# Performance work log

Hardware: AMD Instinct MI355X
Metric: run time of the kernel (lower is better)

The kernel has to match this reference:

```python
import jax, jax.numpy as jnp
import numpy as np
import math

B, L, D, H = 2, 2048, 1024, 16
HD = D // H
DILATION, WINDOW, CAUSAL = 2, 512, True
EPS = 1e-5  # nn.LayerNorm default


def _ln(x, g, b):
    mu = x.mean(-1, keepdims=True)
    var = ((x - mu) ** 2).mean(-1, keepdims=True)
    return (x - mu) * jax.lax.rsqrt(var + EPS) * g + b


def setup_inputs() -> dict:
    key = jax.random.key(0)
    ks = jax.random.split(key, 8)
    s = 0.02  # small init scale to keep activations sane
    return {
        'x': jax.random.normal(ks[0], (B, L, D), jnp.float32),
        'ln1_g': jnp.ones((D,), jnp.float32),
        'ln1_b': jnp.zeros((D,), jnp.float32),
        'Wqkv': jax.random.normal(ks[1], (D, 3 * D), jnp.float32) * s,
        'bqkv': jnp.zeros((3 * D,), jnp.float32),
        'Wout': jax.random.normal(ks[2], (D, D), jnp.float32) * s,
        'bout': jnp.zeros((D,), jnp.float32),
        'ln2_g': jnp.ones((D,), jnp.float32),
        'ln2_b': jnp.zeros((D,), jnp.float32),
        'W1': jax.random.normal(ks[3], (D, 4 * D), jnp.float32) * s,
        'b1': jnp.zeros((4 * D,), jnp.float32),
        'W2': jax.random.normal(ks[4], (4 * D, D), jnp.float32) * s,
        'b2': jnp.zeros((D,), jnp.float32),
    }


def _keep_mask():
    # True = allowed. Matches _build_dilated_keep_mask.
    idx = jnp.arange(L, dtype=jnp.int32)
    delta = idx[:, None] - idx[None, :]
    keep = (jnp.remainder(delta, DILATION) == 0)
    keep = keep & (jnp.abs(delta) <= WINDOW)
    if CAUSAL:
        keep = keep & (delta >= 0)
    return keep  # [L, L]


def reference(x, ln1_g, ln1_b, Wqkv, bqkv, Wout, bout, ln2_g, ln2_b, W1, b1, W2, b2):
    # --- attention sub-block (pre-norm) ---
    h = _ln(x, ln1_g, ln1_b)                          # [B,L,D]
    qkv = (h @ Wqkv + bqkv).reshape(B, L, 3, H, HD)
    q = qkv[:, :, 0].transpose(0, 2, 1, 3)            # [B,H,L,HD]
    k = qkv[:, :, 1].transpose(0, 2, 1, 3)
    v = qkv[:, :, 2].transpose(0, 2, 1, 3)
    scale = 1.0 / math.sqrt(HD)
    scores = jnp.einsum('bhqd,bhkd->bhqk', q, k) * scale
    keep = _keep_mask()                               # [L,L] broadcast over B,H
    scores = jnp.where(keep, scores, jnp.float32(-1e30))
    attn = jax.nn.softmax(scores, axis=-1)
    o = jnp.einsum('bhqk,bhkd->bhqd', attn, v)        # [B,H,L,HD]
    o = o.transpose(0, 2, 1, 3).reshape(B, L, D)
    x = x + (o @ Wout + bout)
    # --- FFN sub-block (pre-norm) ---
    h2 = _ln(x, ln2_g, ln2_b)
    f = jax.nn.gelu(h2 @ W1 + b1, approximate=False)  # nn.GELU default = exact
    x = x + (f @ W2 + b2)
    return x
```

## Files before the change

kernel.cpp:

```cpp
#include <hip/hip_runtime.h>

typedef unsigned short u16;
typedef short short8 __attribute__((ext_vector_type(8)));
typedef float floatx4 __attribute__((ext_vector_type(4)));

#define B_  2
#define L_  2048
#define D_  1024
#define H_  16
#define HD_ 64
#define M_  (B_*L_)
#define LP_ 1024
#define WP_ 256

__device__ __forceinline__ float b2f(u16 u) {
    union { unsigned int i; float f; } c; c.i = ((unsigned int)u) << 16; return c.f;
}
__device__ __forceinline__ u16 f2b(float f) {
    union { float f; unsigned int i; } c; c.f = f;
    unsigned int u = c.i;
    u = u + 0x7FFFu + ((u >> 16) & 1u);
    return (u16)(u >> 16);
}
__device__ __forceinline__ float ldrawf(const void* p, size_t i, bool isbf16) {
    return isbf16 ? b2f(((const u16*)p)[i]) : ((const float*)p)[i];
}
__device__ __forceinline__ u16 ldraw16(const void* p, size_t i, bool isbf16) {
    return isbf16 ? ((const u16*)p)[i] : f2b(((const float*)p)[i]);
}

__global__ void probe_k(const u16* x, int* flag) {
    int t = threadIdx.x;
    unsigned int u = x[2 * t];
    unsigned int e = (u >> 7) & 0xFF;
    bool sane = (e >= 100 && e <= 140);
    unsigned long long m = __ballot(sane);
    if (t == 0) *flag = (__popcll(m) >= 32) ? 1 : 0;
}

__global__ __launch_bounds__(256) void transpose_k(const void* __restrict__ in,
                                                   u16* __restrict__ out, int K, int N,
                                                   const int* flagp) {
    bool isb = (*flagp != 0);
    __shared__ u16 tile[32][33];
    int tx = threadIdx.x & 31;
    int ty = threadIdx.x >> 5;
    int nb = blockIdx.x * 32;
    int kb = blockIdx.y * 32;
    #pragma unroll
    for (int j = 0; j < 32; j += 8)
        tile[ty + j][tx] = ldraw16(in, (size_t)(kb + ty + j) * N + nb + tx, isb);
    __syncthreads();
    #pragma unroll
    for (int j = 0; j < 32; j += 8)
        out[(size_t)(nb + ty + j) * K + kb + tx] = tile[tx][ty + j];
}

template<int SRC>
__global__ __launch_bounds__(256) void ln_k(const void* __restrict__ x, const void* __restrict__ g,
                                            const void* __restrict__ bb, u16* __restrict__ out,
                                            const int* flagp) {
    bool isb = (*flagp != 0);
    int row = blockIdx.x;
    int t = threadIdx.x;
    float v[4]; float s = 0.f, s2 = 0.f;
    #pragma unroll
    for (int i = 0; i < 4; i++) {
        size_t idx = (size_t)row * D_ + t + 256 * i;
        float f = (SRC == 1) ? ((const float*)x)[idx] : ldrawf(x, idx, isb);
        v[i] = f; s += f; s2 += f * f;
    }
    #pragma unroll
    for (int off = 32; off >= 1; off >>= 1) { s += __shfl_xor(s, off); s2 += __shfl_xor(s2, off); }
    __shared__ float red[8];
    int wave = t >> 6;
    if ((t & 63) == 0) { red[wave] = s; red[4 + wave] = s2; }
    __syncthreads();
    s  = red[0] + red[1] + red[2] + red[3];
    s2 = red[4] + red[5] + red[6] + red[7];
    float mu  = s * (1.0f / 1024.0f);
    float var = s2 * (1.0f / 1024.0f) - mu * mu;
    float rs  = rsqrtf(var + 1e-5f);
    #pragma unroll
    for (int i = 0; i < 4; i++) {
        int c = t + 256 * i;
        out[(size_t)row * D_ + c] = f2b((v[i] - mu) * rs * ldrawf(g, c, isb) + ldrawf(bb, c, isb));
    }
}

template<int OUT, int RES, int GELU>
__global__ __launch_bounds__(256) void gemm_k(const u16* __restrict__ A,
                                              const u16* __restrict__ BT,
                                              const void* __restrict__ bias,
                                              const void* __restrict__ resid,
                                              void* __restrict__ C,
                                              int M, int N, int K,
                                              const int* flagp) {
    bool isb = (*flagp != 0);
    __shared__ __align__(16) u16 a_s[64 * 40];
    __shared__ __align__(16) u16 b_s[64 * 40];

    const int bm = blockIdx.y, bn = blockIdx.x;
    const int t = threadIdx.x;
    const int wave = t >> 6, lane = t & 63;
    const int wm = wave >> 1, wn = wave & 1;
    const int quad = lane >> 4, r16 = lane & 15;

    const int srow = t >> 2;
    const int scol = (t & 3) * 8;

    floatx4 acc[2][2] = {};

    const u16* Ap  = A  + (size_t)(bm * 64 + srow) * K + scol;
    const u16* BTp = BT + (size_t)(bn * 64 + srow) * K + scol;

    for (int kc = 0; kc < K; kc += 32) {
        int4 av = *(const int4*)(Ap + kc);
        int4 bv = *(const int4*)(BTp + kc);
        __syncthreads();
        *(int4*)(a_s + srow * 40 + scol) = av;
        *(int4*)(b_s + srow * 40 + scol) = bv;
        __syncthreads();
        short8 af0 = *(const short8*)(a_s + (wm * 32 +      r16) * 40 + quad * 8);
        short8 af1 = *(const short8*)(a_s + (wm * 32 + 16 + r16) * 40 + quad * 8);
        short8 bf0 = *(const short8*)(b_s + (wn * 32 +      r16) * 40 + quad * 8);
        short8 bf1 = *(const short8*)(b_s + (wn * 32 + 16 + r16) * 40 + quad * 8);
        acc[0][0] = __builtin_amdgcn_mfma_f32_16x16x32_bf16(af0, bf0, acc[0][0], 0, 0, 0);
        acc[0][1] = __builtin_amdgcn_mfma_f32_16x16x32_bf16(af0, bf1, acc[0][1], 0, 0, 0);
        acc[1][0] = __builtin_amdgcn_mfma_f32_16x16x32_bf16(af1, bf0, acc[1][0], 0, 0, 0);
        acc[1][1] = __builtin_amdgcn_mfma_f32_16x16x32_bf16(af1, bf1, acc[1][1], 0, 0, 0);
    }

    #pragma unroll
    for (int mt = 0; mt < 2; mt++)
      #pragma unroll
      for (int nt = 0; nt < 2; nt++)
        #pragma unroll
        for (int r = 0; r < 4; r++) {
            int row = bm * 64 + wm * 32 + mt * 16 + quad * 4 + r;
            int col = bn * 64 + wn * 32 + nt * 16 + r16;
            float v = acc[mt][nt][r] + ldrawf(bias, col, isb);
            if (GELU) v = 0.5f * v * (1.0f + erff(v * 0.70710678118654752f));
            if (RES == 1) v += ldrawf(resid, (size_t)row * N + col, isb);
            if (RES == 2) v += ((const float*)resid)[(size_t)row * N + col];
            size_t oi = (size_t)row * N + col;
            if (OUT == 0) ((float*)C)[oi] = v;
            else if (OUT == 1) ((u16*)C)[oi] = f2b(v);
            else {
                if (isb) ((u16*)C)[oi] = f2b(v);
                else     ((float*)C)[oi] = v;
            }
        }
}

__global__ __launch_bounds__(256) void repack_k(const u16* __restrict__ qkv,
                                                u16* __restrict__ Qp, u16* __restrict__ Kp,
                                                u16* __restrict__ Vt) {
    int pid = blockIdx.x;
    int lt  = blockIdx.y;
    int b = pid >> 5, p = (pid >> 4) & 1, h = pid & 15;
    int t = threadIdx.x;
    int srow = t >> 2;
    int scol = (t & 3) * 16;

    int lp = lt * 64 + srow;
    int l  = 2 * lp + p;
    const u16* src = qkv + ((size_t)b * L_ + l) * (3 * D_) + h * HD_;
    size_t dst = ((size_t)pid * LP_ + lp) * HD_;

    *(int4*)(Qp + dst + scol)     = *(const int4*)(src + scol);
    *(int4*)(Qp + dst + scol + 8) = *(const int4*)(src + scol + 8);
    *(int4*)(Kp + dst + scol)     = *(const int4*)(src + D_ + scol);
    *(int4*)(Kp + dst + scol + 8) = *(const int4*)(src + D_ + scol + 8);

    __shared__ u16 vt[64][72];
    *(int4*)(&vt[srow][scol])     = *(const int4*)(src + 2 * D_ + scol);
    *(int4*)(&vt[srow][scol + 8]) = *(const int4*)(src + 2 * D_ + scol + 8);
    __syncthreads();
    union { u16 s[16]; int4 v[2]; } tmp;
    #pragma unroll
    for (int jj = 0; jj < 16; jj++) tmp.s[jj] = vt[scol + jj][srow];
    u16* vdst = Vt + ((size_t)pid * HD_ + srow) * LP_ + lt * 64 + scol;
    *(int4*)(vdst)     = tmp.v[0];
    *(int4*)(vdst + 8) = tmp.v[1];
}

#define FS 72
__global__ __launch_bounds__(256) void fattn_k(const u16* __restrict__ Qp,
                                               const u16* __restrict__ Kp,
                                               const u16* __restrict__ Vt,
                                               u16* __restrict__ o) {
    __shared__ __align__(16) u16 Qs[64 * FS];
    __shared__ __align__(16) u16 Ks[64 * FS];
    __shared__ __align__(16) u16 Vs[64 * FS];
    __shared__ __align__(16) u16 Ps[4][16 * FS];

    const int pid = blockIdx.x, qt = blockIdx.y;
    const int b = pid >> 5, p = (pid >> 4) & 1, h = pid & 15;
    const int t = threadIdx.x, w = t >> 6, lane = t & 63;
    const int quad = lane >> 4, r16 = lane & 15;
    const int q0 = qt * 64;

    const int srow = t >> 2;
    const int scol = (t & 3) * 16;

    const u16* qsrc = Qp + ((size_t)pid * LP_ + q0 + srow) * HD_;
    *(int4*)(Qs + srow * FS + scol)     = *(const int4*)(qsrc + scol);
    *(int4*)(Qs + srow * FS + scol + 8) = *(const int4*)(qsrc + scol + 8);
    __syncthreads();

    const short8 qf0 = *(const short8*)(Qs + (w * 16 + r16) * FS + quad * 8);
    const short8 qf1 = *(const short8*)(Qs + (w * 16 + r16) * FS + quad * 8 + 32);

    floatx4 oacc[4] = {};
    float mrow[4] = {-INFINITY, -INFINITY, -INFINITY, -INFINITY};
    float lrow[4] = {};

    const int kt0 = (qt >= 4) ? qt - 4 : 0;
    const int qrow_base = q0 + w * 16 + quad * 4;

    for (int kt = kt0; kt <= qt; ++kt) {
        __syncthreads();
        const u16* ksrc = Kp + ((size_t)pid * LP_ + kt * 64 + srow) * HD_;
        *(int4*)(Ks + srow * FS + scol)     = *(const int4*)(ksrc + scol);
        *(int4*)(Ks + srow * FS + scol + 8) = *(const int4*)(ksrc + scol + 8);
        const u16* vsrc = Vt + ((size_t)pid * HD_ + srow) * LP_ + kt * 64;
        *(int4*)(Vs + srow * FS + scol)     = *(const int4*)(vsrc + scol);
        *(int4*)(Vs + srow * FS + scol + 8) = *(const int4*)(vsrc + scol + 8);
        __syncthreads();

        floatx4 s4[4];
        #pragma unroll
        for (int nt = 0; nt < 4; nt++) {
            short8 kf0 = *(const short8*)(Ks + (nt * 16 + r16) * FS + quad * 8);
            short8 kf1 = *(const short8*)(Ks + (nt * 16 + r16) * FS + quad * 8 + 32);
            floatx4 z = {};
            z = __builtin_amdgcn_mfma_f32_16x16x32_bf16(qf0, kf0, z, 0, 0, 0);
            z = __builtin_amdgcn_mfma_f32_16x16x32_bf16(qf1, kf1, z, 0, 0, 0);
            s4[nt] = z;
        }

        float sv[4][4];
        #pragma unroll
        for (int nt = 0; nt < 4; nt++) {
            int kcol = kt * 64 + nt * 16 + r16;
            #pragma unroll
            for (int r = 0; r < 4; r++) {
                int kq = kcol - (qrow_base + r);
                bool valid = (kq <= 0) && (kq >= -WP_);
                sv[nt][r] = valid ? s4[nt][r] * 0.125f : -1e30f;
            }
        }

        float mx[4];
        #pragma unroll
        for (int r = 0; r < 4; r++)
            mx[r] = fmaxf(fmaxf(sv[0][r], sv[1][r]), fmaxf(sv[2][r], sv[3][r]));
        #pragma unroll
        for (int off = 8; off >= 1; off >>= 1)
            #pragma unroll
            for (int r = 0; r < 4; r++) mx[r] = fmaxf(mx[r], __shfl_xor(mx[r], off));

        float al[4];
        #pragma unroll
        for (int r = 0; r < 4; r++) {
            float mnew = fmaxf(mrow[r], mx[r]);
            al[r] = __expf(mrow[r] - mnew);
            mrow[r] = mnew;
        }

        float ps[4][4], rs[4] = {};
        #pragma unroll
        for (int nt = 0; nt < 4; nt++)
            #pragma unroll
            for (int r = 0; r < 4; r++) {
                float pv = __expf(sv[nt][r] - mrow[r]);
                ps[nt][r] = pv; rs[r] += pv;
            }
        #pragma unroll
        for (int off = 8; off >= 1; off >>= 1)
            #pragma unroll
            for (int r = 0; r < 4; r++) rs[r] += __shfl_xor(rs[r], off);
        #pragma unroll
        for (int r = 0; r < 4; r++) lrow[r] = lrow[r] * al[r] + rs[r];
        #pragma unroll
        for (int nt = 0; nt < 4; nt++)
            #pragma unroll
            for (int r = 0; r < 4; r++) oacc[nt][r] *= al[r];

        #pragma unroll
        for (int nt = 0; nt < 4; nt++)
            #pragma unroll
            for (int r = 0; r < 4; r++)
                Ps[w][(quad * 4 + r) * FS + nt * 16 + r16] = f2b(ps[nt][r]);
        short8 pf0 = *(const short8*)(&Ps[w][r16 * FS + quad * 8]);
        short8 pf1 = *(const short8*)(&Ps[w][r16 * FS + quad * 8 + 32]);

        #pragma unroll
        for (int nt = 0; nt < 4; nt++) {
            short8 vf0 = *(const short8*)(Vs + (nt * 16 + r16) * FS + quad * 8);
            short8 vf1 = *(const short8*)(Vs + (nt * 16 + r16) * FS + quad * 8 + 32);
            oacc[nt] = __builtin_amdgcn_mfma_f32_16x16x32_bf16(pf0, vf0, oacc[nt], 0, 0, 0);
            oacc[nt] = __builtin_amdgcn_mfma_f32_16x16x32_bf16(pf1, vf1, oacc[nt], 0, 0, 0);
        }
    }

    float inv[4];
    #pragma unroll
    for (int r = 0; r < 4; r++) inv[r] = 1.0f / lrow[r];
    #pragma unroll
    for (int nt = 0; nt < 4; nt++)
        #pragma unroll
        for (int r = 0; r < 4; r++) {
            int qp = qrow_base + r;
            int l  = 2 * qp + p;
            int d  = nt * 16 + r16;
            o[((size_t)b * L_ + l) * D_ + h * HD_ + d] = f2b(oacc[nt][r] * inv[r]);
        }
}

extern "C" void kernel_launch(void* const* d_in, const int* in_sizes, int n_in,
                              void* d_out, int out_size, void* d_ws, size_t ws_size,
                              hipStream_t stream) {
    (void)in_sizes; (void)n_in; (void)out_size; (void)ws_size;
    const void* x     = d_in[0];
    const void* ln1_g = d_in[1];
    const void* ln1_b = d_in[2];
    const void* Wqkv  = d_in[3];
    const void* bqkv  = d_in[4];
    const void* Wout  = d_in[5];
    const void* bout  = d_in[6];
    const void* ln2_g = d_in[7];
    const void* ln2_b = d_in[8];
    const void* W1    = d_in[9];
    const void* b1    = d_in[10];
    const void* W2    = d_in[11];
    const void* b2    = d_in[12];

    char* ws = (char*)d_ws;
    const size_t MB = 1024 * 1024;
    u16*   wqkvT = (u16*)ws;
    u16*   qkv   = (u16*)(ws + 6  * MB);
    u16*   woutT = (u16*)(ws + 30 * MB);
    u16*   fbuf  = (u16*)ws;
    u16*   w1T   = (u16*)(ws + 32 * MB);
    u16*   w2T   = (u16*)(ws + 40 * MB);
    u16*   bufA  = (u16*)(ws + 48 * MB);
    float* x1    = (float*)(ws + 56 * MB);
    u16*   Qp    = (u16*)(ws + 72 * MB);
    u16*   Kp    = (u16*)(ws + 80 * MB);
    u16*   Vt    = (u16*)(ws + 88 * MB);
    int*   flag  = (int*)(ws + 96 * MB);

    dim3 tb(256);
    probe_k<<<1, 64, 0, stream>>>((const u16*)x, flag);

    transpose_k<<<dim3(3 * D_ / 32, D_ / 32), tb, 0, stream>>>(Wqkv, wqkvT, D_, 3 * D_, flag);
    transpose_k<<<dim3(D_ / 32, D_ / 32), tb, 0, stream>>>(Wout, woutT, D_, D_, flag);
    transpose_k<<<dim3(4 * D_ / 32, D_ / 32), tb, 0, stream>>>(W1, w1T, D_, 4 * D_, flag);
    transpose_k<<<dim3(D_ / 32, 4 * D_ / 32), tb, 0, stream>>>(W2, w2T, 4 * D_, D_, flag);

    ln_k<0><<<M_, tb, 0, stream>>>(x, ln1_g, ln1_b, bufA, flag);

    gemm_k<1, 0, 0><<<dim3(3 * D_ / 64, M_ / 64), tb, 0, stream>>>(bufA, wqkvT, bqkv, nullptr, qkv, M_, 3 * D_, D_, flag);

    repack_k<<<dim3(64, 16), tb, 0, stream>>>(qkv, Qp, Kp, Vt);
    fattn_k<<<dim3(64, 16), tb, 0, stream>>>(Qp, Kp, Vt, bufA);

    gemm_k<0, 1, 0><<<dim3(D_ / 64, M_ / 64), tb, 0, stream>>>(bufA, woutT, bout, x, x1, M_, D_, D_, flag);

    ln_k<1><<<M_, tb, 0, stream>>>(x1, ln2_g, ln2_b, bufA, flag);

    gemm_k<1, 0, 1><<<dim3(4 * D_ / 64, M_ / 64), tb, 0, stream>>>(bufA, w1T, b1, nullptr, fbuf, M_, 4 * D_, D_, flag);

    gemm_k<2, 2, 0><<<dim3(D_ / 64, M_ / 64), tb, 0, stream>>>(fbuf, w2T, b2, x1, d_out, M_, D_, 4 * D_, flag);
}
```

Measured before the change: 435.2 us.

## Use larger 128-row GEMM tiles with direct global-to-LDS loads and XOR swizzle

Replaces the 64x64 GEMM with a templated 128xTN kernel (TN of 128 or 64). Each wave now computes a 64xTN/2 sub-tile with up to 16 MFMAs per K step, which raises data reuse per LDS load. Tiles are filled with global_load_lds direct-to-LDS transfers instead of register staging, and the LDS layout uses an XOR swizzle in place of padding to avoid bank conflicts. The cost is fewer blocks for the smaller GEMMs and more accumulator registers per thread. There is still no double buffering, so loads and MFMAs stay serialized by the barriers.

Result: faster. 424.2 us (-2.5%).

```diff
diff --git a/kernel.cpp b/kernel.cpp
--- a/kernel.cpp
+++ b/kernel.cpp
@@ -27,6 +27,11 @@
 }
 __device__ __forceinline__ u16 ldraw16(const void* p, size_t i, bool isbf16) {
     return isbf16 ? ((const u16*)p)[i] : f2b(((const float*)p)[i]);
+}
+__device__ __forceinline__ void gload16(const u16* g, u16* l) {
+    __builtin_amdgcn_global_load_lds(
+        (__attribute__((address_space(1))) void*)(g),
+        (__attribute__((address_space(3))) void*)(l), 16, 0, 0);
 }
 
 __global__ void probe_k(const u16* x, int* flag) {
@@ -88,57 +93,68 @@
     }
 }
 
-template<int OUT, int RES, int GELU>
-__global__ __launch_bounds__(256) void gemm_k(const u16* __restrict__ A,
-                                              const u16* __restrict__ BT,
-                                              const void* __restrict__ bias,
-                                              const void* __restrict__ resid,
-                                              void* __restrict__ C,
-                                              int M, int N, int K,
-                                              const int* flagp) {
+template<int NT, int OUT, int RES, int GELU>
+__global__ __launch_bounds__(256) void gemm128_k(const u16* __restrict__ A,
+                                                 const u16* __restrict__ BT,
+                                                 const void* __restrict__ bias,
+                                                 const void* __restrict__ resid,
+                                                 void* __restrict__ C,
+                                                 int M, int N, int K,
+                                                 const int* flagp) {
+    constexpr int TN = NT * 32;
+    __shared__ __align__(16) u16 a_s[128 * 32];
+    __shared__ __align__(16) u16 b_s[TN * 32];
     bool isb = (*flagp != 0);
-    __shared__ __align__(16) u16 a_s[64 * 40];
-    __shared__ __align__(16) u16 b_s[64 * 40];
 
     const int bm = blockIdx.y, bn = blockIdx.x;
-    const int t = threadIdx.x;
-    const int wave = t >> 6, lane = t & 63;
-    const int wm = wave >> 1, wn = wave & 1;
+    const int t = threadIdx.x, w = t >> 6, lane = t & 63;
+    const int wm = w >> 1, wn = w & 1;
     const int quad = lane >> 4, r16 = lane & 15;
 
-    const int srow = t >> 2;
-    const int scol = (t & 3) * 8;
-
-    floatx4 acc[2][2] = {};
-
-    const u16* Ap  = A  + (size_t)(bm * 64 + srow) * K + scol;
-    const u16* BTp = BT + (size_t)(bn * 64 + srow) * K + scol;
+    const int lr  = lane >> 2;
+    const int lcg = (((lane & 3) ^ ((lr >> 1) & 3))) * 8;
+    const u16* Ag0 = A  + (size_t)(bm * 128 + w * 32 + lr) * K + lcg;
+    const u16* Ag1 = Ag0 + (size_t)16 * K;
+    u16* Al0 = a_s + (w * 32 + lr) * 32 + (lane & 3) * 8;
+    u16* Al1 = Al0 + 16 * 32;
+    const u16* Bg0 = BT + (size_t)(bn * TN + w * (TN / 4) + lr) * K + lcg;
+    const u16* Bg1 = Bg0 + (size_t)16 * K;
+    u16* Bl0 = b_s + (w * (TN / 4) + lr) * 32 + (lane & 3) * 8;
+    u16* Bl1 = Bl0 + 16 * 32;
+
+    const int sw = ((r16 >> 1) & 3);
+    floatx4 acc[4][NT] = {};
 
     for (int kc = 0; kc < K; kc += 32) {
-        int4 av = *(const int4*)(Ap + kc);
-        int4 bv = *(const int4*)(BTp + kc);
         __syncthreads();
-        *(int4*)(a_s + srow * 40 + scol) = av;
-        *(int4*)(b_s + srow * 40 + scol) = bv;
+        gload16(Ag0 + kc, Al0);
+        gload16(Ag1 + kc, Al1);
+        gload16(Bg0 + kc, Bl0);
+        if constexpr (NT == 4) gload16(Bg1 + kc, Bl1);
         __syncthreads();
-        short8 af0 = *(const short8*)(a_s + (wm * 32 +      r16) * 40 + quad * 8);
-        short8 af1 = *(const short8*)(a_s + (wm * 32 + 16 + r16) * 40 + quad * 8);
-        short8 bf0 = *(const short8*)(b_s + (wn * 32 +      r16) * 40 + quad * 8);
-        short8 bf1 = *(const short8*)(b_s + (wn * 32 + 16 + r16) * 40 + quad * 8);
-        acc[0][0] = __builtin_amdgcn_mfma_f32_16x16x32_bf16(af0, bf0, acc[0][0], 0, 0, 0);
-        acc[0][1] = __builtin_amdgcn_mfma_f32_16x16x32_bf16(af0, bf1, acc[0][1], 0, 0, 0);
-        acc[1][0] = __builtin_amdgcn_mfma_f32_16x16x32_bf16(af1, bf0, acc[1][0], 0, 0, 0);
-        acc[1][1] = __builtin_amdgcn_mfma_f32_16x16x32_bf16(af1, bf1, acc[1][1], 0, 0, 0);
+
+        short8 af[4], bf[NT];
+        #pragma unroll
+        for (int mt = 0; mt < 4; mt++)
+            af[mt] = *(const short8*)(a_s + (wm * 64 + mt * 16 + r16) * 32 + (quad ^ sw) * 8);
+        #pragma unroll
+        for (int nt = 0; nt < NT; nt++)
+            bf[nt] = *(const short8*)(b_s + (wn * (TN / 2) + nt * 16 + r16) * 32 + (quad ^ sw) * 8);
+        #pragma unroll
+        for (int mt = 0; mt < 4; mt++)
+            #pragma unroll
+            for (int nt = 0; nt < NT; nt++)
+                acc[mt][nt] = __builtin_amdgcn_mfma_f32_16x16x32_bf16(af[mt], bf[nt], acc[mt][nt], 0, 0, 0);
     }
 
     #pragma unroll
-    for (int mt = 0; mt < 2; mt++)
+    for (int mt = 0; mt < 4; mt++)
       #pragma unroll
-      for (int nt = 0; nt < 2; nt++)
+      for (int nt = 0; nt < NT; nt++)
         #pragma unroll
         for (int r = 0; r < 4; r++) {
-            int row = bm * 64 + wm * 32 + mt * 16 + quad * 4 + r;
-            int col = bn * 64 + wn * 32 + nt * 16 + r16;
+            int row = bm * 128 + wm * 64 + mt * 16 + quad * 4 + r;
+            int col = bn * TN + wn * (TN / 2) + nt * 16 + r16;
             float v = acc[mt][nt][r] + ldrawf(bias, col, isb);
             if (GELU) v = 0.5f * v * (1.0f + erff(v * 0.70710678118654752f));
             if (RES == 1) v += ldrawf(resid, (size_t)row * N + col, isb);
@@ -362,16 +378,16 @@
 
     ln_k<0><<<M_, tb, 0, stream>>>(x, ln1_g, ln1_b, bufA, flag);
 
-    gemm_k<1, 0, 0><<<dim3(3 * D_ / 64, M_ / 64), tb, 0, stream>>>(bufA, wqkvT, bqkv, nullptr, qkv, M_, 3 * D_, D_, flag);
+    gemm128_k<4, 1, 0, 0><<<dim3(3 * D_ / 128, M_ / 128), tb, 0, stream>>>(bufA, wqkvT, bqkv, nullptr, qkv, M_, 3 * D_, D_, flag);
 
     repack_k<<<dim3(64, 16), tb, 0, stream>>>(qkv, Qp, Kp, Vt);
     fattn_k<<<dim3(64, 16), tb, 0, stream>>>(Qp, Kp, Vt, bufA);
 
-    gemm_k<0, 1, 0><<<dim3(D_ / 64, M_ / 64), tb, 0, stream>>>(bufA, woutT, bout, x, x1, M_, D_, D_, flag);
+    gemm128_k<2, 0, 1, 0><<<dim3(D_ / 64, M_ / 128), tb, 0, stream>>>(bufA, woutT, bout, x, x1, M_, D_, D_, flag);
 
     ln_k<1><<<M_, tb, 0, stream>>>(x1, ln2_g, ln2_b, bufA, flag);
 
-    gemm_k<1, 0, 1><<<dim3(4 * D_ / 64, M_ / 64), tb, 0, stream>>>(bufA, w1T, b1, nullptr, fbuf, M_, 4 * D_, D_, flag);
-
-    gemm_k<2, 2, 0><<<dim3(D_ / 64, M_ / 64), tb, 0, stream>>>(fbuf, w2T, b2, x1, d_out, M_, D_, 4 * D_, flag);
-}
+    gemm128_k<4, 1, 0, 1><<<dim3(4 * D_ / 128, M_ / 128), tb, 0, stream>>>(bufA, w1T, b1, nullptr, fbuf, M_, 4 * D_, D_, flag);
+
+    gemm128_k<2, 2, 2, 0><<<dim3(D_ / 64, M_ / 128), tb, 0, stream>>>(fbuf, w2T, b2, x1, d_out, M_, D_, 4 * D_, flag);
+}
```
